# Kernel tuning notes

Hardware: AMD Instinct MI355X
Metric: run time of the kernel (lower is better)

The kernel has to match this reference:

```python
import jax, jax.numpy as jnp
import numpy as np

B, L, D, H = 2, 2048, 2048, 16
HD = D // H  # head_dim = 128
EPS = 1e-5


def setup_inputs() -> dict:
    key = jax.random.key(0)
    ks = jax.random.split(key, 5)
    return {
        "x": jax.random.normal(ks[0], (B, L, D), dtype=jnp.float32),
        "Wq": jax.random.normal(ks[1], (D, D), dtype=jnp.float32) * (D ** -0.5),
        "Wk": jax.random.normal(ks[2], (D, D), dtype=jnp.float32) * (D ** -0.5),
        "Wv": jax.random.normal(ks[3], (D, D), dtype=jnp.float32) * (D ** -0.5),
        "gamma_logit": jax.random.normal(ks[4], (H,), dtype=jnp.float32),
        "gn_weight": jnp.ones((D,), dtype=jnp.float32),
        "gn_bias": jnp.zeros((D,), dtype=jnp.float32),
    }


def reference(x, Wq, Wk, Wv, gamma_logit, gn_weight, gn_bias):
    scale = HD ** -0.5
    # projections (torch Linear: y = x @ W.T)
    Q = jnp.einsum('bld,ed->ble', x, Wq).reshape(B, L, H, HD).transpose(0, 2, 1, 3)
    K = jnp.einsum('bld,ed->ble', x, Wk).reshape(B, L, H, HD).transpose(0, 2, 1, 3)
    V = jnp.einsum('bld,ed->ble', x, Wv).reshape(B, L, H, HD).transpose(0, 2, 1, 3)
    # causal exponential decay matrix D[h,i,j] = gamma_h^(i-j), lower-triangular
    pos = jnp.arange(L)
    dist = jnp.abs(pos[None, :] - pos[:, None]).astype(jnp.float32)  # [L,L]
    gamma = jax.nn.sigmoid(gamma_logit)  # [H]
    Dmat = jnp.tril(gamma[:, None, None] ** dist[None, :, :])  # [H,L,L]
    # decayed linear attention (no softmax)
    attn = jnp.einsum('bhid,bhjd->bhij', Q, K) * scale * Dmat[None]
    out = jnp.einsum('bhij,bhje->bhie', attn, V)  # [B,H,L,HD]
    out = out.transpose(0, 2, 1, 3)  # [B,L,H,HD]
    # GroupNorm: channels=D, groups=H, spatial=L -> normalize per (b,h) over (L,HD)
    mean = out.mean(axis=(1, 3), keepdims=True)
    var = out.var(axis=(1, 3), keepdims=True)
    y = (out - mean) * jax.lax.rsqrt(var + EPS)
    y = y * gn_weight.reshape(1, 1, H, HD) + gn_bias.reshape(1, 1, H, HD)
    return y.reshape(B, L, D)
```

## Files before the change

### kernel.cpp

```cpp
#include <hip/hip_runtime.h>
#include <hip/hip_bf16.h>
#include <math.h>

#define B_  2
#define L_  2048
#define D_  2048
#define H_  16
#define HD_ 128
#define EPS_ 1e-5f
#define NTK 32

typedef __attribute__((ext_vector_type(8)))  short short8;
typedef __attribute__((ext_vector_type(4)))  float f32x4;
typedef __attribute__((ext_vector_type(16))) float f32x16;

static __device__ inline unsigned short bfb(float x) {
    __hip_bfloat16 h = __float2bfloat16(x);
    unsigned short s;
    __builtin_memcpy(&s, &h, 2);
    return s;
}
static __device__ inline unsigned pk2(float a, float b) {
    return (unsigned)bfb(a) | ((unsigned)bfb(b) << 16);
}
static __device__ inline float bf2f(unsigned short u) {
    unsigned v = ((unsigned)u) << 16;
    float f;
    __builtin_memcpy(&f, &v, 4);
    return f;
}

static __device__ __forceinline__ void gld_lds16(const void* g, void* l) {
    __builtin_amdgcn_global_load_lds(
        (const __attribute__((address_space(1))) unsigned int*)g,
        (__attribute__((address_space(3))) unsigned int*)l,
        16, 0, 0);
}

#define XN4 2097152
#define WN4 1048576
#define TOT4 (XN4 + 3 * WN4)

__global__ __launch_bounds__(256) void cast4_kernel(
    const float* __restrict__ x,  const float* __restrict__ Wq,
    const float* __restrict__ Wk, const float* __restrict__ Wv,
    __hip_bfloat16* __restrict__ dst)
{
    int i = blockIdx.x * 256 + threadIdx.x;
    const int st = gridDim.x * 256;
    for (; i < TOT4; i += st) {
        const float* s;
        int off;
        if (i < XN4)                { s = x;  off = i; }
        else if (i < XN4 + WN4)     { s = Wq; off = i - XN4; }
        else if (i < XN4 + 2 * WN4) { s = Wk; off = i - XN4 - WN4; }
        else                        { s = Wv; off = i - XN4 - 2 * WN4; }
        float4 v = ((const float4*)s)[off];
        uint2 r;
        r.x = pk2(v.x, v.y);
        r.y = pk2(v.z, v.w);
        ((uint2*)dst)[i] = r;
    }
}

__global__ __launch_bounds__(512) void proj8(
    const __hip_bfloat16* __restrict__ X,
    const __hip_bfloat16* __restrict__ Wc,
    __hip_bfloat16* __restrict__ Qo, __hip_bfloat16* __restrict__ Ko,
    __hip_bfloat16* __restrict__ VT, __hip_bfloat16* __restrict__ KT)
{
    __shared__ __align__(16) char lds[98304];

    const int t  = threadIdx.x;
    const int w  = t >> 6, l = t & 63;
    const int li = l & 15, hi4 = l >> 4;
    const int wm = w >> 2, wn = w & 3;

    const int bid = blockIdx.x;
    const int wg  = (bid & 7) * 96 + (bid >> 3);
    const int nt  = wg >> 5;
    const int mt  = wg & 31;
    const int m0  = mt * 128;
    const int n0g = nt * 256;

    const int srow = l >> 3;
    const int scol = ((l & 7) ^ (l >> 3)) * 8;
    const int ca0  = 2 * w;
    const int cb0  = 4 * w;

    f32x4 acc[4][4];
    #pragma unroll
    for (int i = 0; i < 4; ++i)
        #pragma unroll
        for (int j = 0; j < 4; ++j)
            #pragma unroll
            for (int r = 0; r < 4; ++r) acc[i][j][r] = 0.f;

    auto STAGE_A = [&](int tt) {
        char* Ab = lds + (tt & 1) * 16384;
        char* Bb = lds + 32768 + (tt & 1) * 32768;
        const size_t kc = (size_t)(tt * 64) + scol;
        gld_lds16(X  + (size_t)(m0 + ca0 * 8 + srow) * D_ + kc,      Ab + ca0 * 1024);
        gld_lds16(X  + (size_t)(m0 + ca0 * 8 + 8 + srow) * D_ + kc,  Ab + ca0 * 1024 + 1024);
        gld_lds16(Wc + (size_t)(n0g + cb0 * 8 + srow) * D_ + kc,     Bb + cb0 * 1024);
    };
    auto STAGE_B = [&](int tt) {
        char* Bb = lds + 32768 + (tt & 1) * 32768;
        const size_t kc = (size_t)(tt * 64) + scol;
        gld_lds16(Wc + (size_t)(n0g + (cb0 + 1) * 8 + srow) * D_ + kc, Bb + (cb0 + 1) * 1024);
        gld_lds16(Wc + (size_t)(n0g + (cb0 + 2) * 8 + srow) * D_ + kc, Bb + (cb0 + 2) * 1024);
        gld_lds16(Wc + (size_t)(n0g + (cb0 + 3) * 8 + srow) * D_ + kc, Bb + (cb0 + 3) * 1024);
    };

    STAGE_A(0); STAGE_B(0); STAGE_A(1); STAGE_B(1);

    const int cbk0 = (hi4 * 16) ^ ((li & 7) << 4);
    const int cbk1 = (64 + hi4 * 16) ^ ((li & 7) << 4);

    #pragma unroll 2
    for (int kt = 0; kt < NTK; ++kt) {
        const char* Ab = lds + (kt & 1) * 16384;
        const char* Bb = lds + 32768 + (kt & 1) * 32768;

        if (kt < NTK - 1) asm volatile("s_waitcnt vmcnt(6)" ::: "memory");
        else              asm volatile("s_waitcnt vmcnt(0)" ::: "memory");
        __builtin_amdgcn_s_barrier();

        short8 a0[4], b0[4], a1[4], b1[4];
        #pragma unroll
        for (int mf = 0; mf < 4; ++mf)
            a0[mf] = *(const short8*)(Ab + (wm * 64 + mf * 16 + li) * 128 + cbk0);
        #pragma unroll
        for (int nf = 0; nf < 4; ++nf)
            b0[nf] = *(const short8*)(Bb + (wn * 64 + nf * 16 + li) * 128 + cbk0);
        __builtin_amdgcn_s_setprio(1);
        #pragma unroll
        for (int mf = 0; mf < 4; ++mf)
            #pragma unroll
            for (int nf = 0; nf < 2; ++nf)
                acc[mf][nf] = __builtin_amdgcn_mfma_f32_16x16x32_bf16(
                    a0[mf], b0[nf], acc[mf][nf], 0, 0, 0);
        __builtin_amdgcn_s_setprio(0);

        #pragma unroll
        for (int mf = 0; mf < 4; ++mf)
            a1[mf] = *(const short8*)(Ab + (wm * 64 + mf * 16 + li) * 128 + cbk1);
        #pragma unroll
        for (int nf = 0; nf < 4; ++nf)
            b1[nf] = *(const short8*)(Bb + (wn * 64 + nf * 16 + li) * 128 + cbk1);
        __builtin_amdgcn_s_setprio(1);
        #pragma unroll
        for (int mf = 0; mf < 4; ++mf)
            #pragma unroll
            for (int nf = 2; nf < 4; ++nf)
                acc[mf][nf] = __builtin_amdgcn_mfma_f32_16x16x32_bf16(
                    a0[mf], b0[nf], acc[mf][nf], 0, 0, 0);
        __builtin_amdgcn_s_setprio(0);

        asm volatile("s_waitcnt lgkmcnt(0)" ::: "memory");
        __builtin_amdgcn_s_barrier();

        if (kt < NTK - 2) STAGE_A(kt + 2);
        __builtin_amdgcn_s_setprio(1);
        #pragma unroll
        for (int mf = 0; mf < 4; ++mf)
            #pragma unroll
            for (int nf = 0; nf < 2; ++nf)
                acc[mf][nf] = __builtin_amdgcn_mfma_f32_16x16x32_bf16(
                    a1[mf], b1[nf], acc[mf][nf], 0, 0, 0);
        __builtin_amdgcn_s_setprio(0);

        if (kt < NTK - 2) STAGE_B(kt + 2);
        __builtin_amdgcn_s_setprio(1);
        #pragma unroll
        for (int mf = 0; mf < 4; ++mf)
            #pragma unroll
            for (int nf = 2; nf < 4; ++nf)
                acc[mf][nf] = __builtin_amdgcn_mfma_f32_16x16x32_bf16(
                    a1[mf], b1[nf], acc[mf][nf], 0, 0, 0);
        __builtin_amdgcn_s_setprio(0);
    }

    const int zsel = n0g >> 11;
    const int np   = n0g & (D_ - 1);
    if (zsel == 2) {
        #pragma unroll
        for (int mf = 0; mf < 4; ++mf) {
            #pragma unroll
            for (int nf = 0; nf < 4; ++nf) {
                const int n     = np + wn * 64 + nf * 16 + li;
                const int mbase = m0 + wm * 64 + mf * 16 + hi4 * 4;
                const int b = mbase >> 11, ml = mbase & (L_ - 1);
                uint2 w2;
                w2.x = pk2(acc[mf][nf][0], acc[mf][nf][1]);
                w2.y = pk2(acc[mf][nf][2], acc[mf][nf][3]);
                *(uint2*)&VT[((size_t)b * D_ + n) * L_ + ml] = w2;
            }
        }
    } else {
        __hip_bfloat16* O = zsel ? Ko : Qo;
        #pragma unroll
        for (int mf = 0; mf < 4; ++mf) {
            #pragma unroll
            for (int nf = 0; nf < 4; ++nf) {
                const int n  = np + wn * 64 + nf * 16 + li;
                const int h  = n >> 7, hd = n & (HD_ - 1);
                #pragma unroll
                for (int r = 0; r < 4; ++r) {
                    const int m = m0 + wm * 64 + mf * 16 + hi4 * 4 + r;
                    const int b = m >> 11, ml = m & (L_ - 1);
                    O[((size_t)(b * H_ + h) * L_ + ml) * HD_ + hd] =
                        __float2bfloat16(acc[mf][nf][r]);
                }
            }
        }
        if (zsel == 1 && KT != nullptr) {
            #pragma unroll
            for (int mf = 0; mf < 4; ++mf) {
                #pragma unroll
                for (int nf = 0; nf < 4; ++nf) {
                    const int n     = np + wn * 64 + nf * 16 + li;
                    const int mbase = m0 + wm * 64 + mf * 16 + hi4 * 4;
                    const int b = mbase >> 11, ml = mbase & (L_ - 1);
                    uint2 w2;
                    w2.x = pk2(acc[mf][nf][0], acc[mf][nf][1]);
                    w2.y = pk2(acc[mf][nf][2], acc[mf][nf][3]);
                    *(uint2*)&KT[((size_t)b * D_ + n) * L_ + ml] = w2;
                }
            }
        }
    }
}

__global__ __launch_bounds__(256) void state_part(
    const __hip_bfloat16* __restrict__ KT, const __hip_bfloat16* __restrict__ VT,
    const float* __restrict__ gl, __hip_bfloat16* __restrict__ SpT)
{
    const int bid = blockIdx.x;
    const int bh  = bid & 31, c = bid >> 5;
    const int h   = bh & (H_ - 1);
    const int t   = threadIdx.x;
    const int w   = t >> 6, l = t & 63;
    const int li  = l & 31, hi = l >> 5;

    const float gamma = 1.f / (1.f + __expf(-gl[h]));
    const float lg2   = __log2f(gamma);

    __shared__ __align__(16) char Kl[32768];
    __shared__ __align__(16) char Vl[32768];

    const __hip_bfloat16* KTg = KT + (size_t)bh * (HD_ * L_);
    const __hip_bfloat16* VTg = VT + (size_t)bh * (HD_ * L_);
    const int gj = c * 128;
    const int srow4 = l >> 4, sslot = l & 15;

    #pragma unroll
    for (int cc = 0; cc < 8; ++cc) {
        const int ch = w * 8 + cc;
        const int r  = ch * 4 + srow4;
        const int sc = ((sslot ^ (r & 15)) * 8);
        gld_lds16(KTg + (size_t)r * L_ + gj + sc, Kl + ch * 1024);
        gld_lds16(VTg + (size_t)r * L_ + gj + sc, Vl + ch * 1024);
    }
    __syncthreads();

    f32x16 acc[4];
    #pragma unroll
    for (int cch = 0; cch < 4; ++cch)
        #pragma unroll
        for (int r = 0; r < 16; ++r) acc[cch][r] = 0.f;

    #pragma unroll
    for (int s = 0; s < 8; ++s) {
        const int boff = ((s * 2 + hi) ^ (li & 15)) << 4;
        short8 vraw = *(const short8*)(Vl + (w * 32 + li) * 256 + boff);
        short8 af;
        #pragma unroll
        for (int e = 0; e < 8; ++e) {
            const int jl = s * 16 + hi * 8 + e;
            const float f = bf2f((unsigned short)vraw[e]) *
                            exp2f(lg2 * (float)(127 - jl));
            af[e] = (short)bfb(f);
        }
        __builtin_amdgcn_s_setprio(1);
        #pragma unroll
        for (int cch = 0; cch < 4; ++cch) {
            short8 bf = *(const short8*)(Kl + (cch * 32 + li) * 256 + boff);
            acc[cch] = __builtin_amdgcn_mfma_f32_32x32x16_bf16(af, bf, acc[cch], 0, 0, 0);
        }
        __builtin_amdgcn_s_setprio(0);
    }

    __hip_bfloat16* Sp = SpT + (size_t)(bh * 16 + c) * 16384;
    #pragma unroll
    for (int cch = 0; cch < 4; ++cch)
        #pragma unroll
        for (int r = 0; r < 16; ++r) {
            const int d = w * 32 + (r & 3) + 8 * (r >> 2) + 4 * hi;
            Sp[(size_t)d * 128 + cch * 32 + li] = __float2bfloat16(acc[cch][r]);
        }
}

__global__ __launch_bounds__(256) void state_scan(
    const __hip_bfloat16* __restrict__ SpT, __hip_bfloat16* __restrict__ SbT,
    const float* __restrict__ gl)
{
    const int bh = blockIdx.x;
    const int h  = bh & (H_ - 1);
    const float gamma = 1.f / (1.f + __expf(-gl[h]));
    const float g128  = exp2f(__log2f(gamma) * 128.f);
    const int fid = blockIdx.y * 256 + threadIdx.x;

    float a0 = 0.f, a1 = 0.f, a2 = 0.f, a3 = 0.f;
    for (int c = 0; c < 16; ++c) {
        const size_t off = (size_t)(bh * 16 + c) * 16384 + (size_t)fid * 4;
        uint2 v = *(const uint2*)(SpT + off);
        a0 = g128 * a0 + bf2f((unsigned short)(v.x & 0xffff));
        a1 = g128 * a1 + bf2f((unsigned short)(v.x >> 16));
        a2 = g128 * a2 + bf2f((unsigned short)(v.y & 0xffff));
        a3 = g128 * a3 + bf2f((unsigned short)(v.y >> 16));
        uint2 o;
        o.x = pk2(a0, a1);
        o.y = pk2(a2, a3);
        *(uint2*)(SbT + off) = o;
    }
}

__global__ __launch_bounds__(256) void retn_kernel(
    const __hip_bfloat16* __restrict__ Qb, const __hip_bfloat16* __restrict__ Kb,
    const __hip_bfloat16* __restrict__ VT, const float* __restrict__ gl,
    float* __restrict__ out, float2* __restrict__ part,
    const __hip_bfloat16* __restrict__ SbT, int use_chunks)
{
    const int bid = blockIdx.x;
    const int mm  = bid >> 5;
    const int m   = use_chunks ? mm : ((mm < 8) ? (15 - mm) : (mm - 8));
    const int bh  = bid & 31;
    const int b   = bh >> 4, h = bh & (H_ - 1);
    const int t   = threadIdx.x;
    const int w   = t >> 6, l = t & 63;
    const int li  = l & 31, hi = l >> 5;

    const float gamma = 1.f / (1.f + __expf(-gl[h]));
    const float lg2   = __log2f(gamma);
    const float scale = 0.08838834764831845f;

    __shared__ __align__(16) char Klds[32768];
    __shared__ __align__(16) char Vlds[32768];
    __shared__ float rs[4], rq[4];

    const size_t base = (size_t)bh * (L_ * HD_);
    const __hip_bfloat16* VTg = VT + (size_t)bh * (HD_ * L_);
    const int i0 = m * 128 + w * 32;

    short8 qf[8];
    {
        const __hip_bfloat16* qrow = Qb + base + (size_t)(i0 + li) * HD_;
        #pragma unroll
        for (int s = 0; s < 8; ++s)
            qf[s] = *(const short8*)(qrow + s * 16 + hi * 8);
    }

    float df[16];
    #pragma unroll
    for (int r = 0; r < 16; ++r) {
        const int jl = (r & 3) + 8 * (r >> 2) + 4 * hi;
        df[r] = exp2f(lg2 * (float)(li - jl));
    }

    f32x16 acc[4];
    #pragma unroll
    for (int c = 0; c < 4; ++c)
        #pragma unroll
        for (int r = 0; r < 16; ++r) acc[c][r] = 0.f;

    const int srow4 = l >> 4;
    const int sslot = l & 15;

    if (use_chunks && m > 0) {
        const __hip_bfloat16* Sg = SbT + (size_t)(bh * 16 + (m - 1)) * 16384;
        #pragma unroll
        for (int cc = 0; cc < 8; ++cc) {
            const int ch = w * 8 + cc;
            const int r  = ch * 4 + srow4;
            const int sc = ((sslot ^ (r & 15)) * 8);
            gld_lds16(Sg + (size_t)r * 128 + sc, Klds + ch * 1024);
        }
        __syncthreads();
        #pragma unroll
        for (int s = 0; s < 8; ++s) {
            const int boff = ((s * 2 + hi) ^ (li & 15)) << 4;
            __builtin_amdgcn_s_setprio(1);
            #pragma unroll
            for (int cch = 0; cch < 4; ++cch) {
                short8 sf = *(const short8*)(Klds + (cch * 32 + li) * 256 + boff);
                acc[cch] = __builtin_amdgcn_mfma_f32_32x32x16_bf16(
                    qf[s], sf, acc[cch], 0, 0, 0);
            }
            __builtin_amdgcn_s_setprio(0);
        }
        #pragma unroll
        for (int r = 0; r < 16; ++r) {
            const int il = (r & 3) + 8 * (r >> 2) + 4 * hi + w * 32;
            const float fr = exp2f(lg2 * (float)(il + 1)) * scale;
            acc[0][r] *= fr; acc[1][r] *= fr; acc[2][r] *= fr; acc[3][r] *= fr;
        }
    }

    const int gj0 = use_chunks ? m * 128 : 0;
    for (int gj = gj0; gj <= m * 128; gj += 128) {
        __syncthreads();
        #pragma unroll
        for (int cc = 0; cc < 8; ++cc) {
            const int c  = w * 8 + cc;
            const int r  = c * 4 + srow4;
            const int sc = ((sslot ^ (r & 15)) * 8);
            gld_lds16(Kb + base + (size_t)(gj + r) * HD_ + sc, Klds + c * 1024);
            gld_lds16(VTg + (size_t)r * L_ + gj + sc,          Vlds + c * 1024);
        }
        __syncthreads();

        const int tmax = ((i0 - gj) >> 5) < 3 ? ((i0 - gj) >> 5) : 3;
        for (int jt = 0; jt <= tmax; ++jt) {
            const int j0 = gj + jt * 32;

            f32x16 c;
            #pragma unroll
            for (int r = 0; r < 16; ++r) c[r] = 0.f;
            __builtin_amdgcn_s_setprio(1);
            #pragma unroll
            for (int s = 0; s < 8; ++s) {
                short8 kf = *(const short8*)(Klds + (jt * 32 + li) * 256 +
                                             (((s * 2 + hi) ^ (li & 15)) << 4));
                c = __builtin_amdgcn_mfma_f32_32x32x16_bf16(kf, qf[s], c, 0, 0, 0);
            }
            __builtin_amdgcn_s_setprio(0);

            float p[16];
            const float bt = exp2f(lg2 * (float)(i0 - j0)) * scale;
            if (j0 == i0) {
                #pragma unroll
                for (int r = 0; r < 16; ++r) {
                    const int jl = (r & 3) + 8 * (r >> 2) + 4 * hi;
                    p[r] = (jl <= li) ? c[r] * (df[r] * bt) : 0.f;
                }
            } else {
                #pragma unroll
                for (int r = 0; r < 16; ++r) p[r] = c[r] * (df[r] * bt);
            }

            #pragma unroll
            for (int sl = 0; sl < 2; ++sl) {
                const int o = sl * 8;
                unsigned pk01 = pk2(p[o + 0], p[o + 1]);
                unsigned pk23 = pk2(p[o + 2], p[o + 3]);
                unsigned pk45 = pk2(p[o + 4], p[o + 5]);
                unsigned pk67 = pk2(p[o + 6], p[o + 7]);
                unsigned x01 = (unsigned)__shfl_xor((int)pk01, 32);
                unsigned x23 = (unsigned)__shfl_xor((int)pk23, 32);
                unsigned x45 = (unsigned)__shfl_xor((int)pk45, 32);
                unsigned x67 = (unsigned)__shfl_xor((int)pk67, 32);
                union { short8 v; unsigned u[4]; } pf;
                pf.u[0] = hi ? x45 : pk01;
                pf.u[1] = hi ? x67 : pk23;
                pf.u[2] = hi ? pk45 : x01;
                pf.u[3] = hi ? pk67 : x23;
                __builtin_amdgcn_s_setprio(1);
                #pragma unroll
                for (int cch = 0; cch < 4; ++cch) {
                    short8 vf = *(const short8*)(Vlds + (cch * 32 + li) * 256 +
                                 (((jt * 4 + sl * 2 + hi) ^ (li & 15)) << 4));
                    acc[cch] = __builtin_amdgcn_mfma_f32_32x32x16_bf16(
                        pf.v, vf, acc[cch], 0, 0, 0);
                }
                __builtin_amdgcn_s_setprio(0);
            }
        }
    }

    float s = 0.f, sq = 0.f;
    #pragma unroll
    for (int cch = 0; cch < 4; ++cch) {
        #pragma unroll
        for (int r = 0; r < 16; ++r) {
            const int row = (r & 3) + 8 * (r >> 2) + 4 * hi;
            const float v = acc[cch][r];
            out[(size_t)(b * L_ + i0 + row) * D_ + h * HD_ + cch * 32 + li] = v;
            s += v; sq += v * v;
        }
    }

    #pragma unroll
    for (int off = 32; off > 0; off >>= 1) {
        s  += __shfl_down(s, off);
        sq += __shfl_down(sq, off);
    }
    if (l == 0) { rs[w] = s; rq[w] = sq; }
    __syncthreads();
    if (t == 0)
        part[bh * 16 + m] = make_float2(rs[0] + rs[1] + rs[2] + rs[3],
                                        rq[0] + rq[1] + rq[2] + rq[3]);
}

__global__ __launch_bounds__(256) void gn_apply(
    float* __restrict__ out, const float2* __restrict__ part,
    const float* __restrict__ gw, const float* __restrict__ gb)
{
    const int bh = blockIdx.x, sl = blockIdx.y;
    const int b = bh >> 4, h = bh & (H_ - 1);
    const int t = threadIdx.x;

    float S = 0.f, SQ = 0.f;
    #pragma unroll
    for (int i = 0; i < 16; ++i) {
        float2 p = part[bh * 16 + i];
        S += p.x; SQ += p.y;
    }
    const float inv  = 1.f / (float)(L_ * HD_);
    const float mean = S * inv;
    float var = SQ * inv - mean * mean;
    if (var < 0.f) var = 0.f;
    const float rstd = rsqrtf(var + EPS_);

    #pragma unroll
    for (int it = 0; it < 4; ++it) {
        const int n  = it * 256 + t;
        const int ll = n >> 5, d4 = n & 31;
        const size_t idx = (size_t)(b * L_ + sl * 32 + ll) * D_ + h * HD_ + d4 * 4;
        float4 v = *(const float4*)&out[idx];
        const float4 w4 = *(const float4*)&gw[h * HD_ + d4 * 4];
        const float4 b4 = *(const float4*)&gb[h * HD_ + d4 * 4];
        v.x = (v.x - mean) * rstd * w4.x + b4.x;
        v.y = (v.y - mean) * rstd * w4.y + b4.y;
        v.z = (v.z - mean) * rstd * w4.z + b4.z;
        v.w = (v.w - mean) * rstd * w4.w + b4.w;
        *(float4*)&out[idx] = v;
    }
}

extern "C" void kernel_launch(void* const* d_in, const int* in_sizes, int n_in,
                              void* d_out, int out_size, void* d_ws, size_t ws_size,
                              hipStream_t stream) {
    const float* x  = (const float*)d_in[0];
    const float* Wq = (const float*)d_in[1];
    const float* Wk = (const float*)d_in[2];
    const float* Wv = (const float*)d_in[3];
    const float* gl = (const float*)d_in[4];
    const float* gw = (const float*)d_in[5];
    const float* gb = (const float*)d_in[6];
    float* out = (float*)d_out;

    __hip_bfloat16* ws = (__hip_bfloat16*)d_ws;
    __hip_bfloat16* xb  = ws;
    __hip_bfloat16* Wqb = xb  + 8388608;
    __hip_bfloat16* Wkb = Wqb + 4194304;
    __hip_bfloat16* Wvb = Wkb + 4194304;
    __hip_bfloat16* Qbf = Wvb + 4194304;
    __hip_bfloat16* Kbf = Qbf + 8388608;
    __hip_bfloat16* VTb = Kbf + 8388608;
    float2* part = (float2*)(VTb + 8388608);
    __hip_bfloat16* KTb = (__hip_bfloat16*)(part + 512);

    __hip_bfloat16* SpT = xb;
    __hip_bfloat16* SbT = Wqb;

    const int use_chunks = (ws_size >= 109056000ULL) ? 1 : 0;

    cast4_kernel<<<2048, 256, 0, stream>>>(x, Wq, Wk, Wv, xb);

    proj8<<<dim3(768), 512, 0, stream>>>(xb, Wqb, Qbf, Kbf, VTb,
                                         use_chunks ? KTb : nullptr);

    if (use_chunks) {
        state_part<<<dim3(512), 256, 0, stream>>>(KTb, VTb, gl, SpT);
        state_scan<<<dim3(32, 16), 256, 0, stream>>>(SpT, SbT, gl);
    }

    retn_kernel<<<dim3(512), 256, 0, stream>>>(Qbf, Kbf, VTb, gl, out, part,
                                               use_chunks ? SbT : nullptr,
                                               use_chunks);

    gn_apply<<<dim3(32, 64), 256, 0, stream>>>(out, part, gw, gb);
}
```

Baseline: 185.0 us.

## Enlarge projection GEMM tile to 256x256 with restaged LDS pipeline

Measured after the change: 200.5 us. +8.4%, slower.

```diff
diff --git a/kernel.cpp b/kernel.cpp
--- a/kernel.cpp
+++ b/kernel.cpp
@@ -8,7 +8,7 @@
 #define H_  16
 #define HD_ 128
 #define EPS_ 1e-5f
-#define NTK 32
+#define NT2 32
 
 typedef __attribute__((ext_vector_type(8)))  short short8;
 typedef __attribute__((ext_vector_type(4)))  float f32x4;
@@ -63,13 +63,13 @@
     }
 }
 
-__global__ __launch_bounds__(512) void proj8(
+__global__ __launch_bounds__(512) void proj256(
     const __hip_bfloat16* __restrict__ X,
     const __hip_bfloat16* __restrict__ Wc,
     __hip_bfloat16* __restrict__ Qo, __hip_bfloat16* __restrict__ Ko,
     __hip_bfloat16* __restrict__ VT, __hip_bfloat16* __restrict__ KT)
 {
-    __shared__ __align__(16) char lds[98304];
+    __shared__ __align__(16) char lds[131072];
 
     const int t  = threadIdx.x;
     const int w  = t >> 6, l = t & 63;
@@ -77,107 +77,122 @@
     const int wm = w >> 2, wn = w & 3;
 
     const int bid = blockIdx.x;
-    const int wg  = (bid & 7) * 96 + (bid >> 3);
-    const int nt  = wg >> 5;
-    const int mt  = wg & 31;
-    const int m0  = mt * 128;
+    const int wg  = (bid & 7) * 48 + (bid >> 3);
+    const int nt  = wg >> 4;
+    const int mt  = wg & 15;
+    const int m0  = mt * 256;
     const int n0g = nt * 256;
 
     const int srow = l >> 3;
     const int scol = ((l & 7) ^ (l >> 3)) * 8;
-    const int ca0  = 2 * w;
-    const int cb0  = 4 * w;
-
-    f32x4 acc[4][4];
-    #pragma unroll
-    for (int i = 0; i < 4; ++i)
+    const int swz  = (li & 7) << 4;
+
+    f32x4 acc[8][4];
+    #pragma unroll
+    for (int i = 0; i < 8; ++i)
         #pragma unroll
         for (int j = 0; j < 4; ++j)
             #pragma unroll
             for (int r = 0; r < 4; ++r) acc[i][j][r] = 0.f;
 
+    auto STAGE_B = [&](int tt) {
+        char* Bb = lds + (tt & 1) * 65536 + 32768;
+        const size_t kc = (size_t)(tt * 64) + scol;
+        #pragma unroll
+        for (int j = 0; j < 4; ++j) {
+            const int chunk = w * 4 + j;
+            const int row   = chunk * 8 + srow;
+            gld_lds16(Wc + (size_t)(n0g + row) * D_ + kc, Bb + chunk * 1024);
+        }
+    };
     auto STAGE_A = [&](int tt) {
-        char* Ab = lds + (tt & 1) * 16384;
-        char* Bb = lds + 32768 + (tt & 1) * 32768;
+        char* Ab = lds + (tt & 1) * 65536;
         const size_t kc = (size_t)(tt * 64) + scol;
-        gld_lds16(X  + (size_t)(m0 + ca0 * 8 + srow) * D_ + kc,      Ab + ca0 * 1024);
-        gld_lds16(X  + (size_t)(m0 + ca0 * 8 + 8 + srow) * D_ + kc,  Ab + ca0 * 1024 + 1024);
-        gld_lds16(Wc + (size_t)(n0g + cb0 * 8 + srow) * D_ + kc,     Bb + cb0 * 1024);
+        #pragma unroll
+        for (int j = 0; j < 4; ++j) {
+            const int chunk = w * 4 + j;
+            const int row   = chunk * 8 + srow;
+            gld_lds16(X + (size_t)(m0 + row) * D_ + kc, Ab + chunk * 1024);
+        }
     };
-    auto STAGE_B = [&](int tt) {
-        char* Bb = lds + 32768 + (tt & 1) * 32768;
-        const size_t kc = (size_t)(tt * 64) + scol;
-        gld_lds16(Wc + (size_t)(n0g + (cb0 + 1) * 8 + srow) * D_ + kc, Bb + (cb0 + 1) * 1024);
-        gld_lds16(Wc + (size_t)(n0g + (cb0 + 2) * 8 + srow) * D_ + kc, Bb + (cb0 + 2) * 1024);
-        gld_lds16(Wc + (size_t)(n0g + (cb0 + 3) * 8 + srow) * D_ + kc, Bb + (cb0 + 3) * 1024);
-    };
-
-    STAGE_A(0); STAGE_B(0); STAGE_A(1); STAGE_B(1);
-
-    const int cbk0 = (hi4 * 16) ^ ((li & 7) << 4);
-    const int cbk1 = (64 + hi4 * 16) ^ ((li & 7) << 4);
-
-    #pragma unroll 2
-    for (int kt = 0; kt < NTK; ++kt) {
-        const char* Ab = lds + (kt & 1) * 16384;
-        const char* Bb = lds + 32768 + (kt & 1) * 32768;
-
-        if (kt < NTK - 1) asm volatile("s_waitcnt vmcnt(6)" ::: "memory");
+
+    STAGE_B(0); STAGE_A(0); STAGE_B(1); STAGE_A(1);
+
+    for (int kt = 0; kt < NT2; ++kt) {
+        const char* Ab = lds + (kt & 1) * 65536;
+        const char* Bb = Ab + 32768;
+
+        if (kt < NT2 - 1) asm volatile("s_waitcnt vmcnt(8)" ::: "memory");
         else              asm volatile("s_waitcnt vmcnt(0)" ::: "memory");
+        __builtin_amdgcn_sched_barrier(0);
         __builtin_amdgcn_s_barrier();
-
-        short8 a0[4], b0[4], a1[4], b1[4];
+        __builtin_amdgcn_sched_barrier(0);
+
+        short8 a[4][2], b[4][2], a2[4][2];
         #pragma unroll
         for (int mf = 0; mf < 4; ++mf)
-            a0[mf] = *(const short8*)(Ab + (wm * 64 + mf * 16 + li) * 128 + cbk0);
+            #pragma unroll
+            for (int kk = 0; kk < 2; ++kk)
+                a[mf][kk] = *(const short8*)(Ab + (wm * 128 + mf * 16 + li) * 128 +
+                                             ((kk * 64 + hi4 * 16) ^ swz));
         #pragma unroll
         for (int nf = 0; nf < 4; ++nf)
-            b0[nf] = *(const short8*)(Bb + (wn * 64 + nf * 16 + li) * 128 + cbk0);
+            #pragma unroll
+            for (int kk = 0; kk < 2; ++kk)
+                b[nf][kk] = *(const short8*)(Bb + (wn * 64 + nf * 16 + li) * 128 +
+                                             ((kk * 64 + hi4 * 16) ^ swz));
         __builtin_amdgcn_s_setprio(1);
         #pragma unroll
         for (int mf = 0; mf < 4; ++mf)
             #pragma unroll
-            for (int nf = 0; nf < 2; ++nf)
+            for (int nf = 0; nf < 4; ++nf)
                 acc[mf][nf] = __builtin_amdgcn_mfma_f32_16x16x32_bf16(
-                    a0[mf], b0[nf], acc[mf][nf], 0, 0, 0);
+                    a[mf][0], b[nf][0], acc[mf][nf], 0, 0, 0);
         __builtin_amdgcn_s_setprio(0);
 
+        asm volatile("s_waitcnt lgkmcnt(0)" ::: "memory");
+        __builtin_amdgcn_sched_barrier(0);
+        __builtin_amdgcn_s_barrier();
+        __builtin_amdgcn_sched_barrier(0);
+
+        if (kt < NT2 - 2) STAGE_B(kt + 2);
+        __builtin_amdgcn_s_setprio(1);
         #pragma unroll
         for (int mf = 0; mf < 4; ++mf)
-            a1[mf] = *(const short8*)(Ab + (wm * 64 + mf * 16 + li) * 128 + cbk1);
-        #pragma unroll
-        for (int nf = 0; nf < 4; ++nf)
-            b1[nf] = *(const short8*)(Bb + (wn * 64 + nf * 16 + li) * 128 + cbk1);
+            #pragma unroll
+            for (int nf = 0; nf < 4; ++nf)
+                acc[mf][nf] = __builtin_amdgcn_mfma_f32_16x16x32_bf16(
+                    a[mf][1], b[nf][1], acc[mf][nf], 0, 0, 0);
+        __builtin_amdgcn_s_setprio(0);
+
+        #pragma unroll
+        for (int mf = 0; mf < 4; ++mf)
+            #pragma unroll
+            for (int kk = 0; kk < 2; ++kk)
+                a2[mf][kk] = *(const short8*)(Ab + (wm * 128 + (mf + 4) * 16 + li) * 128 +
+                                              ((kk * 64 + hi4 * 16) ^ swz));
         __builtin_amdgcn_s_setprio(1);
         #pragma unroll
         for (int mf = 0; mf < 4; ++mf)
             #pragma unroll
-            for (int nf = 2; nf < 4; ++nf)
-                acc[mf][nf] = __builtin_amdgcn_mfma_f32_16x16x32_bf16(
-                    a0[mf], b0[nf], acc[mf][nf], 0, 0, 0);
+            for (int nf = 0; nf < 4; ++nf)
+                acc[mf + 4][nf] = __builtin_amdgcn_mfma_f32_16x16x32_bf16(
+                    a2[mf][0], b[nf][0], acc[mf + 4][nf], 0, 0, 0);
         __builtin_amdgcn_s_setprio(0);
 
         asm volatile("s_waitcnt lgkmcnt(0)" ::: "memory");
+        __builtin_amdgcn_sched_barrier(0);
         __builtin_amdgcn_s_barrier();
-
-        if (kt < NTK - 2) STAGE_A(kt + 2);
+        __builtin_amdgcn_sched_barrier(0);
+
+        if (kt < NT2 - 2) STAGE_A(kt + 2);
         __builtin_amdgcn_s_setprio(1);
         #pragma unroll
         for (int mf = 0; mf < 4; ++mf)
             #pragma unroll
-            for (int nf = 0; nf < 2; ++nf)
-                acc[mf][nf] = __builtin_amdgcn_mfma_f32_16x16x32_bf16(
-                    a1[mf], b1[nf], acc[mf][nf], 0, 0, 0);
-        __builtin_amdgcn_s_setprio(0);
-
-        if (kt < NTK - 2) STAGE_B(kt + 2);
-        __builtin_amdgcn_s_setprio(1);
-        #pragma unroll
-        for (int mf = 0; mf < 4; ++mf)
-            #pragma unroll
-            for (int nf = 2; nf < 4; ++nf)
-                acc[mf][nf] = __builtin_amdgcn_mfma_f32_16x16x32_bf16(
-                    a1[mf], b1[nf], acc[mf][nf], 0, 0, 0);
+            for (int nf = 0; nf < 4; ++nf)
+                acc[mf + 4][nf] = __builtin_amdgcn_mfma_f32_16x16x32_bf16(
+                    a2[mf][1], b[nf][1], acc[mf + 4][nf], 0, 0, 0);
         __builtin_amdgcn_s_setprio(0);
     }
 
@@ -185,11 +200,11 @@
     const int np   = n0g & (D_ - 1);
     if (zsel == 2) {
         #pragma unroll
-        for (int mf = 0; mf < 4; ++mf) {
+        for (int mf = 0; mf < 8; ++mf) {
             #pragma unroll
             for (int nf = 0; nf < 4; ++nf) {
                 const int n     = np + wn * 64 + nf * 16 + li;
-                const int mbase = m0 + wm * 64 + mf * 16 + hi4 * 4;
+                const int mbase = m0 + wm * 128 + mf * 16 + hi4 * 4;
                 const int b = mbase >> 11, ml = mbase & (L_ - 1);
                 uint2 w2;
                 w2.x = pk2(acc[mf][nf][0], acc[mf][nf][1]);
@@ -200,14 +215,14 @@
     } else {
         __hip_bfloat16* O = zsel ? Ko : Qo;
         #pragma unroll
-        for (int mf = 0; mf < 4; ++mf) {
+        for (int mf = 0; mf < 8; ++mf) {
             #pragma unroll
             for (int nf = 0; nf < 4; ++nf) {
                 const int n  = np + wn * 64 + nf * 16 + li;
                 const int h  = n >> 7, hd = n & (HD_ - 1);
                 #pragma unroll
                 for (int r = 0; r < 4; ++r) {
-                    const int m = m0 + wm * 64 + mf * 16 + hi4 * 4 + r;
+                    const int m = m0 + wm * 128 + mf * 16 + hi4 * 4 + r;
                     const int b = m >> 11, ml = m & (L_ - 1);
                     O[((size_t)(b * H_ + h) * L_ + ml) * HD_ + hd] =
                         __float2bfloat16(acc[mf][nf][r]);
@@ -216,11 +231,11 @@
         }
         if (zsel == 1 && KT != nullptr) {
             #pragma unroll
-            for (int mf = 0; mf < 4; ++mf) {
+            for (int mf = 0; mf < 8; ++mf) {
                 #pragma unroll
                 for (int nf = 0; nf < 4; ++nf) {
                     const int n     = np + wn * 64 + nf * 16 + li;
-                    const int mbase = m0 + wm * 64 + mf * 16 + hi4 * 4;
+                    const int mbase = m0 + wm * 128 + mf * 16 + hi4 * 4;
                     const int b = mbase >> 11, ml = mbase & (L_ - 1);
                     uint2 w2;
                     w2.x = pk2(acc[mf][nf][0], acc[mf][nf][1]);
@@ -568,8 +583,8 @@
 
     cast4_kernel<<<2048, 256, 0, stream>>>(x, Wq, Wk, Wv, xb);
 
-    proj8<<<dim3(768), 512, 0, stream>>>(xb, Wqb, Qbf, Kbf, VTb,
-                                         use_chunks ? KTb : nullptr);
+    proj256<<<dim3(384), 512, 0, stream>>>(xb, Wqb, Qbf, Kbf, VTb,
+                                           use_chunks ? KTb : nullptr);
 
     if (use_chunks) {
         state_part<<<dim3(512), 256, 0, stream>>>(KTb, VTb, gl, SpT);
```
